# Performance work log

Hardware: AMD Instinct MI355X
Metric: run time of the kernel (lower is better)

The kernel has to match this reference:

```python
import jax, jax.numpy as jnp
import numpy as np

B, N = 4096, 128
STATE_DIM, GOAL_DIM, OBSTACLE_DIM = 6, 6, 4
VEH = 2 * STATE_DIM + GOAL_DIM  # 18


def setup_inputs() -> dict:
    key = jax.random.key(0)
    ks = jax.random.split(key, 8)
    s = lambda k, shp, fan: jax.random.normal(k, shp, jnp.float32) / np.sqrt(fan)
    return {
        "obs": jax.random.normal(ks[0], (B, 138), jnp.float32),
        "obstacles": jax.random.uniform(ks[1], (B, 5, N), jnp.float32),
        "act": jax.random.normal(ks[2], (B, 2), jnp.float32),
        "ow1": s(ks[3], (22, 256), 22),
        "ob1": jnp.zeros((256,), jnp.float32),
        "ow2": s(ks[4], (256, 256), 256),
        "ob2": jnp.zeros((256,), jnp.float32),
        "qw1": s(ks[5], (396, 256), 396),
        "qb1": jnp.zeros((256,), jnp.float32),
        "qw2": s(ks[6], (256, 256), 256),
        "qb2": jnp.zeros((256,), jnp.float32),
        "qw3": s(ks[7], (256, 1), 256),
        "qb3": jnp.zeros((1,), jnp.float32),
    }


def reference(obs, obstacles, act, ow1, ob1, ow2, ob2, qw1, qb1, qw2, qb2, qw3, qb3):
    # obs: [B, 138]; obstacles: [B, obstacle_dim+1, N]; act: [B, 2]
    veh = obs[:, :VEH]                                 # [B, 18]
    obst_data = obstacles[:, :OBSTACLE_DIM, :]         # [B, 4, N]
    mask = obstacles[:, -1, :]                         # [B, N]
    # per-obstacle features: concat broadcast vehicle state with obstacle data -> [B, N, 22]
    x = jnp.concatenate(
        [jnp.broadcast_to(veh[:, None, :], (veh.shape[0], obst_data.shape[2], VEH)),
         obst_data.transpose(0, 2, 1)], axis=-1)
    # shared obstacle MLP (ReLU on both layers, incl. output_activation)
    h = jax.nn.relu(jnp.einsum("bnf,fh->bnh", x, ow1) + ob1)
    h = jax.nn.relu(jnp.einsum("bnh,hk->bnk", h, ow2) + ob2)  # [B, N, 256]
    # masked sum-pool over obstacle axis
    pooled = jnp.einsum("bnh,bn->bh", h, mask)         # [B, 256]
    comb = jnp.concatenate([obs, pooled, act], axis=-1)  # [B, 396]
    q = jax.nn.relu(comb @ qw1 + qb1)
    q = jax.nn.relu(q @ qw2 + qb2)
    q = q @ qw3 + qb3                                   # [B, 1]
    return jnp.squeeze(q, -1)
```

## Files before the change

### kernel.cpp

```cpp
#include <hip/hip_runtime.h>
#include <hip/hip_bf16.h>


typedef __attribute__((ext_vector_type(8))) short short8;
typedef __attribute__((ext_vector_type(4))) float f32x4;

#define MFMA16(A, B, C) __builtin_amdgcn_mfma_f32_16x16x32_bf16(A, B, C, 0, 0, 0)

__device__ __forceinline__ unsigned short f2b(float f) {
  __hip_bfloat16 h = __float2bfloat16(f);
  return __builtin_bit_cast(unsigned short, h);
}
__device__ __forceinline__ float b2f(unsigned short u) {
  unsigned v = ((unsigned)u) << 16;
  return __builtin_bit_cast(float, v);
}
__device__ __forceinline__ unsigned pk2f(float a, float b) {
  unsigned ua = __builtin_bit_cast(unsigned, a) + 0x8000u;
  unsigned ub = __builtin_bit_cast(unsigned, b) + 0x8000u;
  return __builtin_amdgcn_perm(ub, ua, 0x07060302u);
}

__device__ __forceinline__ void lds_barrier() {
  asm volatile("s_waitcnt lgkmcnt(0)" ::: "memory");
  __builtin_amdgcn_s_barrier();
}

__global__ __launch_bounds__(256) void pack_weights(
    const float* __restrict__ ow1, const float* __restrict__ ow2,
    const float* __restrict__ qw1, const float* __restrict__ qw2,
    unsigned short* __restrict__ ow1q, unsigned short* __restrict__ ow2p,
    unsigned short* __restrict__ qw1h, unsigned short* __restrict__ qw1l,
    unsigned short* __restrict__ qw2h, unsigned short* __restrict__ qw2l) {
  int i = blockIdx.x * 256 + threadIdx.x;
  if (i < 8192) {
    int j = i & 7;
    int l15 = (i >> 3) & 15;
    int quad = (i >> 7) & 3;
    int mt = (i >> 9) & 15;
    int k = quad * 8 + j;
    float v = (k < 22) ? ow1[k * 256 + (mt * 16 + l15)] : 0.f;
    ow1q[i] = f2b(v);
  }
  if (i < 65536) {
    int j = i & 7;
    int n = (i >> 3) & 255;
    int qq = i >> 11;
    int k = (qq >> 2) * 32 + (qq & 3) * 8 + j;
    ow2p[i] = f2b(ow2[k * 256 + n]);
    float w = qw2[k * 256 + n];
    unsigned short h = f2b(w);
    qw2h[i] = h;
    qw2l[i] = f2b(w - b2f(h));
  }
  if (i < 106496) {
    int j = i & 7;
    int n = (i >> 3) & 255;
    int qq = i >> 11;
    int k = (qq >> 2) * 32 + (qq & 3) * 8 + j;
    float w = (k < 396) ? qw1[k * 256 + n] : 0.f;
    unsigned short h = f2b(w);
    qw1h[i] = h;
    qw1l[i] = f2b(w - b2f(h));
  }
}

#define XSTR 40
#define HSTR 272

__global__ __launch_bounds__(512, 4) void obstacle_kernel(
    const float* __restrict__ obs, const float* __restrict__ obstacles,
    const unsigned short* __restrict__ ow1q,
    const unsigned short* __restrict__ ow2p,
    const float* __restrict__ ob1, const float* __restrict__ ob2,
    unsigned short* __restrict__ poolH, unsigned short* __restrict__ poolL) {
  __shared__ __align__(16) unsigned short xs[128 * XSTR];
  __shared__ __align__(16) unsigned short h1[128 * HSTR];
  __shared__ float maskS[128];
  __shared__ unsigned short vehB[32];

  const int b = blockIdx.x;
  const int tid = threadIdx.x;
  const int wave = tid >> 6;
  const int lane = tid & 63;
  const int quad = lane >> 4;
  const int l15 = lane & 15;

  const unsigned short* wp = &ow1q[wave * 1024 + quad * 128 + l15 * 8];
  short8 wfr[2];
#pragma unroll
  for (int i = 0; i < 2; i++) wfr[i] = *(const short8*)(wp + i * 512);

  const unsigned short* bbase = &ow2p[(quad * 256 + wave * 32 + l15) * 8];
  short8 bbuf[2][2];
#pragma unroll
  for (int t = 0; t < 2; t++)
    bbuf[0][t] = *(const short8*)(bbase + wave * 8192 + t * 128);

  if (tid < 18) vehB[tid] = f2b(obs[b * 138 + tid]);
  if (tid < 128) maskS[tid] = obstacles[b * 640 + 512 + tid];
  lds_barrier();

  if (tid < 256) {
    int n = tid >> 1;
    int half = tid & 1;
    unsigned short* wr = &xs[n * XSTR + half * 16];
    if (half == 0) {
      unsigned short r01[16];
#pragma unroll
      for (int k = 0; k < 16; k++) r01[k] = vehB[k];
      *(short8*)(wr + 0) = *(short8*)&r01[0];
      *(short8*)(wr + 8) = *(short8*)&r01[8];
    } else {
      unsigned short r2[8];
      r2[0] = vehB[16];
      r2[1] = vehB[17];
#pragma unroll
      for (int d = 0; d < 4; d++)
        r2[2 + d] = f2b(obstacles[b * 640 + d * 128 + n]);
      r2[6] = 0; r2[7] = 0;
      *(short8*)(wr + 0) = *(short8*)&r2[0];
      short8 z = {0, 0, 0, 0, 0, 0, 0, 0};
      *(short8*)(wr + 8) = z;
    }
  }
  lds_barrier();

  {
    const unsigned short* bxp = &xs[l15 * XSTR + quad * 8];
    short8 bx[8];
#pragma unroll
    for (int nt = 0; nt < 8; nt++)
      bx[nt] = *(const short8*)(bxp + nt * 16 * XSTR);

    unsigned short* wrb = &h1[l15 * HSTR + wave * 32 + quad * 4];

#pragma unroll
    for (int i = 0; i < 2; i++) {
      f32x4 cinit = *(const f32x4*)&ob1[wave * 32 + i * 16 + quad * 4];
      f32x4 acc1[8];
#pragma unroll
      for (int nt = 0; nt < 8; nt++) acc1[nt] = MFMA16(wfr[i], bx[nt], cinit);
#pragma unroll
      for (int nt = 0; nt < 8; nt++) {
        float v0 = fmaxf(acc1[nt][0], 0.f);
        float v1 = fmaxf(acc1[nt][1], 0.f);
        float v2 = fmaxf(acc1[nt][2], 0.f);
        float v3 = fmaxf(acc1[nt][3], 0.f);
        uint2 pk;
        pk.x = pk2f(v0, v1);
        pk.y = pk2f(v2, v3);
        *(uint2*)(wrb + nt * 16 * HSTR + i * 16) = pk;
      }
    }
  }

  f32x4 acc[8][2];
#pragma unroll
  for (int t = 0; t < 2; t++) {
    float bv = ob2[wave * 32 + t * 16 + l15];
    f32x4 bvec = {bv, bv, bv, bv};
#pragma unroll
    for (int mt = 0; mt < 8; mt++) acc[mt][t] = bvec;
  }

  const unsigned short* h1base = &h1[l15 * HSTR + quad * 8];

  {
    const int kb = wave;
#pragma unroll
    for (int t = 0; t < 2; t++)
      bbuf[1][t] = *(const short8*)(bbase + (((wave + 1) & 7) * 8192) + t * 128);
    short8 afr[8];
#pragma unroll
    for (int mt = 0; mt < 8; mt++)
      afr[mt] = *(const short8*)(h1base + kb * 32 + mt * 16 * HSTR);
#pragma unroll
    for (int mt = 0; mt < 8; mt++)
#pragma unroll
      for (int t = 0; t < 2; t++) acc[mt][t] = MFMA16(afr[mt], bbuf[0][t], acc[mt][t]);
  }

  lds_barrier();

#pragma unroll
  for (int j = 1; j < 8; j++) {
    const int kb = (wave + j) & 7;
    const int cur = j & 1;
    if (j < 7) {
#pragma unroll
      for (int t = 0; t < 2; t++)
        bbuf[cur ^ 1][t] =
            *(const short8*)(bbase + (((wave + j + 1) & 7) * 8192) + t * 128);
    }
    short8 afr[8];
#pragma unroll
    for (int mt = 0; mt < 8; mt++)
      afr[mt] = *(const short8*)(h1base + kb * 32 + mt * 16 * HSTR);
#pragma unroll
    for (int mt = 0; mt < 8; mt++)
#pragma unroll
      for (int t = 0; t < 2; t++) acc[mt][t] = MFMA16(afr[mt], bbuf[cur][t], acc[mt][t]);
  }

  f32x4 mk[8];
  const float* mkp = &maskS[quad * 4];
#pragma unroll
  for (int mt = 0; mt < 8; mt++) mk[mt] = *(const f32x4*)(mkp + mt * 16);

#pragma unroll
  for (int t = 0; t < 2; t++) {
    float s = 0.f;
#pragma unroll
    for (int mt = 0; mt < 8; mt++) {
#pragma unroll
      for (int r = 0; r < 4; r++) {
        float v = fmaxf(acc[mt][t][r], 0.f);
        s = fmaf(mk[mt][r], v, s);
      }
    }
    s += __shfl_xor(s, 16);
    s += __shfl_xor(s, 32);
    if (quad == 0) {
      int n = wave * 32 + t * 16 + l15;
      unsigned short sh = (unsigned short)(__builtin_bit_cast(unsigned, s) >> 16);
      poolH[b * 256 + n] = sh;
      poolL[b * 256 + n] = f2b(s - b2f(sh));
    }
  }
}

__global__ __launch_bounds__(1024) void head_mfma(
    const float* __restrict__ obs, const float* __restrict__ act,
    const unsigned short* __restrict__ poolH,
    const unsigned short* __restrict__ poolL,
    const unsigned short* __restrict__ qw1h,
    const unsigned short* __restrict__ qw1l,
    const unsigned short* __restrict__ qw2h,
    const unsigned short* __restrict__ qw2l,
    const float* __restrict__ qb1, const float* __restrict__ qb2,
    const float* __restrict__ qw3, const float* __restrict__ qb3,
    float* __restrict__ out) {
  const int CSTR = 424;
  const int HSTRQ = 264;
  __shared__ unsigned short combH[16 * 424], combL[16 * 424];
  __shared__ unsigned short h1H[16 * 264], h1L[16 * 264];
  __shared__ float wred[16][16];

  const int tid = threadIdx.x;
  const int r0 = blockIdx.x * 16;

  for (int idx = tid; idx < 16 * 416; idx += 1024) {
    int m = idx / 416;
    int k = idx - m * 416;
    unsigned short hi, lo;
    if (k < 138) {
      float v = obs[(r0 + m) * 138 + k];
      hi = f2b(v);
      lo = f2b(v - b2f(hi));
    } else if (k < 394) {
      hi = poolH[(r0 + m) * 256 + (k - 138)];
      lo = poolL[(r0 + m) * 256 + (k - 138)];
    } else if (k < 396) {
      float v = act[(r0 + m) * 2 + (k - 394)];
      hi = f2b(v);
      lo = f2b(v - b2f(hi));
    } else {
      hi = 0; lo = 0;
    }
    combH[m * CSTR + k] = hi;
    combL[m * CSTR + k] = lo;
  }
  __syncthreads();

  const int wave = tid >> 6;
  const int lane = tid & 63;
  const int quad = lane >> 4;
  const int l15 = lane & 15;
  const int n = wave * 16 + l15;

  f32x4 acc = {0.f, 0.f, 0.f, 0.f}, accm = {0.f, 0.f, 0.f, 0.f};
#pragma unroll 1
  for (int kb = 0; kb < 13; kb++) {
    int ao = l15 * CSTR + kb * 32 + quad * 8;
    short8 ah = *(const short8*)&combH[ao];
    short8 al = *(const short8*)&combL[ao];
    int off = ((kb * 4 + quad) * 256 + n) * 8;
    short8 bh = *(const short8*)&qw1h[off];
    short8 bl = *(const short8*)&qw1l[off];
    acc = MFMA16(ah, bh, acc);
    accm = MFMA16(ah, bl, accm);
    accm = MFMA16(al, bh, accm);
  }
  {
    float bias = qb1[n];
#pragma unroll
    for (int r = 0; r < 4; r++) {
      int m = quad * 4 + r;
      float v = fmaxf(acc[r] + accm[r] + bias, 0.f);
      unsigned short hi = f2b(v);
      h1H[m * HSTRQ + n] = hi;
      h1L[m * HSTRQ + n] = f2b(v - b2f(hi));
    }
  }
  __syncthreads();

  f32x4 a2 = {0.f, 0.f, 0.f, 0.f}, a2m = {0.f, 0.f, 0.f, 0.f};
#pragma unroll 1
  for (int kb = 0; kb < 8; kb++) {
    int ao = l15 * HSTRQ + kb * 32 + quad * 8;
    short8 ah = *(const short8*)&h1H[ao];
    short8 al = *(const short8*)&h1L[ao];
    int off = ((kb * 4 + quad) * 256 + n) * 8;
    short8 bh = *(const short8*)&qw2h[off];
    short8 bl = *(const short8*)&qw2l[off];
    a2 = MFMA16(ah, bh, a2);
    a2m = MFMA16(ah, bl, a2m);
    a2m = MFMA16(al, bh, a2m);
  }

  {
    float w3 = qw3[n];
    float qb2n = qb2[n];
#pragma unroll
    for (int r = 0; r < 4; r++) {
      float v = fmaxf(a2[r] + a2m[r] + qb2n, 0.f);
      float s = v * w3;
      s += __shfl_xor(s, 1);
      s += __shfl_xor(s, 2);
      s += __shfl_xor(s, 4);
      s += __shfl_xor(s, 8);
      if (l15 == 0) wred[wave][quad * 4 + r] = s;
    }
  }
  __syncthreads();
  if (tid < 16) {
    float s = qb3[0];
#pragma unroll
    for (int w = 0; w < 16; w++) s += wred[w][tid];
    out[r0 + tid] = s;
  }
}

extern "C" void kernel_launch(void* const* d_in, const int* in_sizes, int n_in,
                              void* d_out, int out_size, void* d_ws, size_t ws_size,
                              hipStream_t stream) {
  const float* obs       = (const float*)d_in[0];
  const float* obstacles = (const float*)d_in[1];
  const float* act       = (const float*)d_in[2];
  const float* ow1       = (const float*)d_in[3];
  const float* ob1       = (const float*)d_in[4];
  const float* ow2       = (const float*)d_in[5];
  const float* ob2       = (const float*)d_in[6];
  const float* qw1       = (const float*)d_in[7];
  const float* qb1       = (const float*)d_in[8];
  const float* qw2       = (const float*)d_in[9];
  const float* qb2       = (const float*)d_in[10];
  const float* qw3       = (const float*)d_in[11];
  const float* qb3       = (const float*)d_in[12];
  float* out = (float*)d_out;

  unsigned short* ow1q = (unsigned short*)d_ws;
  unsigned short* ow2p = ow1q + 8192;
  unsigned short* qw1h = ow2p + 65536;
  unsigned short* qw1l = qw1h + 106496;
  unsigned short* qw2h = qw1l + 106496;
  unsigned short* qw2l = qw2h + 65536;
  unsigned short* poolH = qw2l + 65536;
  unsigned short* poolL = poolH + 1048576;

  pack_weights<<<416, 256, 0, stream>>>(ow1, ow2, qw1, qw2, ow1q, ow2p, qw1h,
                                        qw1l, qw2h, qw2l);
  obstacle_kernel<<<4096, 512, 0, stream>>>(obs, obstacles, ow1q, ow2p, ob1,
                                            ob2, poolH, poolL);
  head_mfma<<<256, 1024, 0, stream>>>(obs, act, poolH, poolL, qw1h, qw1l,
                                      qw2h, qw2l, qb1, qb2, qw3, qb3, out);
}
```

Baseline: 165.8 us.

## Process two batch rows per obstacle block with register prefetch of next row inputs

Each obstacle_kernel block now handles two consecutive batch elements, halving the grid. The next element's vehicle state, mask and obstacle coordinates are prefetched into registers while the current element's MLP runs, and the layer-1 weight fragments are loaded once and reused across both elements. MFMA sections are wrapped in s_setprio to favour matrix issue. The aim is to hide global-load latency and amortise per-block setup, at the cost of fewer blocks in flight and an extra barrier between elements.

```diff
diff --git a/kernel.cpp b/kernel.cpp
--- a/kernel.cpp
+++ b/kernel.cpp
@@ -79,154 +79,193 @@
   __shared__ float maskS[128];
   __shared__ unsigned short vehB[32];
 
-  const int b = blockIdx.x;
   const int tid = threadIdx.x;
   const int wave = tid >> 6;
   const int lane = tid & 63;
   const int quad = lane >> 4;
   const int l15 = lane & 15;
+  const int b0 = blockIdx.x * 2;
+  const int xn = tid >> 1;
+  const int xhalf = tid & 1;
+
+  float pveh = 0.f, pmask = 0.f, po0 = 0.f, po1 = 0.f, po2 = 0.f, po3 = 0.f;
+  if (tid < 18) pveh = obs[b0 * 138 + tid];
+  if (tid < 128) pmask = obstacles[b0 * 640 + 512 + tid];
+  if (tid < 256 && xhalf) {
+    po0 = obstacles[b0 * 640 + 0 * 128 + xn];
+    po1 = obstacles[b0 * 640 + 1 * 128 + xn];
+    po2 = obstacles[b0 * 640 + 2 * 128 + xn];
+    po3 = obstacles[b0 * 640 + 3 * 128 + xn];
+  }
 
   const unsigned short* wp = &ow1q[wave * 1024 + quad * 128 + l15 * 8];
+  const unsigned short* bbase = &ow2p[(quad * 256 + wave * 32 + l15) * 8];
   short8 wfr[2];
-#pragma unroll
-  for (int i = 0; i < 2; i++) wfr[i] = *(const short8*)(wp + i * 512);
-
-  const unsigned short* bbase = &ow2p[(quad * 256 + wave * 32 + l15) * 8];
-  short8 bbuf[2][2];
-#pragma unroll
-  for (int t = 0; t < 2; t++)
-    bbuf[0][t] = *(const short8*)(bbase + wave * 8192 + t * 128);
-
-  if (tid < 18) vehB[tid] = f2b(obs[b * 138 + tid]);
-  if (tid < 128) maskS[tid] = obstacles[b * 640 + 512 + tid];
-  lds_barrier();
-
-  if (tid < 256) {
-    int n = tid >> 1;
-    int half = tid & 1;
-    unsigned short* wr = &xs[n * XSTR + half * 16];
-    if (half == 0) {
-      unsigned short r01[16];
-#pragma unroll
-      for (int k = 0; k < 16; k++) r01[k] = vehB[k];
-      *(short8*)(wr + 0) = *(short8*)&r01[0];
-      *(short8*)(wr + 8) = *(short8*)&r01[8];
-    } else {
-      unsigned short r2[8];
-      r2[0] = vehB[16];
-      r2[1] = vehB[17];
-#pragma unroll
-      for (int d = 0; d < 4; d++)
-        r2[2 + d] = f2b(obstacles[b * 640 + d * 128 + n]);
-      r2[6] = 0; r2[7] = 0;
-      *(short8*)(wr + 0) = *(short8*)&r2[0];
-      short8 z = {0, 0, 0, 0, 0, 0, 0, 0};
-      *(short8*)(wr + 8) = z;
-    }
-  }
-  lds_barrier();
-
-  {
-    const unsigned short* bxp = &xs[l15 * XSTR + quad * 8];
-    short8 bx[8];
-#pragma unroll
-    for (int nt = 0; nt < 8; nt++)
-      bx[nt] = *(const short8*)(bxp + nt * 16 * XSTR);
-
-    unsigned short* wrb = &h1[l15 * HSTR + wave * 32 + quad * 4];
-
-#pragma unroll
-    for (int i = 0; i < 2; i++) {
-      f32x4 cinit = *(const f32x4*)&ob1[wave * 32 + i * 16 + quad * 4];
-      f32x4 acc1[8];
-#pragma unroll
-      for (int nt = 0; nt < 8; nt++) acc1[nt] = MFMA16(wfr[i], bx[nt], cinit);
-#pragma unroll
-      for (int nt = 0; nt < 8; nt++) {
-        float v0 = fmaxf(acc1[nt][0], 0.f);
-        float v1 = fmaxf(acc1[nt][1], 0.f);
-        float v2 = fmaxf(acc1[nt][2], 0.f);
-        float v3 = fmaxf(acc1[nt][3], 0.f);
-        uint2 pk;
-        pk.x = pk2f(v0, v1);
-        pk.y = pk2f(v2, v3);
-        *(uint2*)(wrb + nt * 16 * HSTR + i * 16) = pk;
-      }
-    }
-  }
-
-  f32x4 acc[8][2];
-#pragma unroll
-  for (int t = 0; t < 2; t++) {
-    float bv = ob2[wave * 32 + t * 16 + l15];
-    f32x4 bvec = {bv, bv, bv, bv};
-#pragma unroll
-    for (int mt = 0; mt < 8; mt++) acc[mt][t] = bvec;
-  }
-
-  const unsigned short* h1base = &h1[l15 * HSTR + quad * 8];
-
-  {
-    const int kb = wave;
+
+#pragma unroll
+  for (int e = 0; e < 2; e++) {
+    const int b = b0 + e;
+
+    if (tid < 18) vehB[tid] = f2b(pveh);
+    if (tid < 128) maskS[tid] = pmask;
+    lds_barrier();
+
+    if (tid < 256) {
+      unsigned short* wr = &xs[xn * XSTR + xhalf * 16];
+      if (xhalf == 0) {
+        unsigned short r01[16];
+#pragma unroll
+        for (int k = 0; k < 16; k++) r01[k] = vehB[k];
+        *(short8*)(wr + 0) = *(short8*)&r01[0];
+        *(short8*)(wr + 8) = *(short8*)&r01[8];
+      } else {
+        unsigned short r2[8];
+        r2[0] = vehB[16];
+        r2[1] = vehB[17];
+        r2[2] = f2b(po0);
+        r2[3] = f2b(po1);
+        r2[4] = f2b(po2);
+        r2[5] = f2b(po3);
+        r2[6] = 0; r2[7] = 0;
+        *(short8*)(wr + 0) = *(short8*)&r2[0];
+        short8 z = {0, 0, 0, 0, 0, 0, 0, 0};
+        *(short8*)(wr + 8) = z;
+      }
+    }
+    lds_barrier();
+
+    if (e == 0) {
+      const int bn = b0 + 1;
+      if (tid < 18) pveh = obs[bn * 138 + tid];
+      if (tid < 128) pmask = obstacles[bn * 640 + 512 + tid];
+      if (tid < 256 && xhalf) {
+        po0 = obstacles[bn * 640 + 0 * 128 + xn];
+        po1 = obstacles[bn * 640 + 1 * 128 + xn];
+        po2 = obstacles[bn * 640 + 2 * 128 + xn];
+        po3 = obstacles[bn * 640 + 3 * 128 + xn];
+      }
+    }
+
+    short8 bbuf[2][2];
 #pragma unroll
     for (int t = 0; t < 2; t++)
-      bbuf[1][t] = *(const short8*)(bbase + (((wave + 1) & 7) * 8192) + t * 128);
-    short8 afr[8];
-#pragma unroll
-    for (int mt = 0; mt < 8; mt++)
-      afr[mt] = *(const short8*)(h1base + kb * 32 + mt * 16 * HSTR);
-#pragma unroll
-    for (int mt = 0; mt < 8; mt++)
-#pragma unroll
-      for (int t = 0; t < 2; t++) acc[mt][t] = MFMA16(afr[mt], bbuf[0][t], acc[mt][t]);
-  }
-
-  lds_barrier();
-
-#pragma unroll
-  for (int j = 1; j < 8; j++) {
-    const int kb = (wave + j) & 7;
-    const int cur = j & 1;
-    if (j < 7) {
+      bbuf[0][t] = *(const short8*)(bbase + wave * 8192 + t * 128);
+
+    {
+      if (e == 0) {
+#pragma unroll
+        for (int i = 0; i < 2; i++) wfr[i] = *(const short8*)(wp + i * 512);
+      }
+
+      const unsigned short* bxp = &xs[l15 * XSTR + quad * 8];
+      short8 bx[8];
+#pragma unroll
+      for (int nt = 0; nt < 8; nt++)
+        bx[nt] = *(const short8*)(bxp + nt * 16 * XSTR);
+
+      unsigned short* wrb = &h1[l15 * HSTR + wave * 32 + quad * 4];
+
+#pragma unroll
+      for (int i = 0; i < 2; i++) {
+        f32x4 cinit = *(const f32x4*)&ob1[wave * 32 + i * 16 + quad * 4];
+        f32x4 acc1[8];
+        __builtin_amdgcn_s_setprio(1);
+#pragma unroll
+        for (int nt = 0; nt < 8; nt++) acc1[nt] = MFMA16(wfr[i], bx[nt], cinit);
+        __builtin_amdgcn_s_setprio(0);
+#pragma unroll
+        for (int nt = 0; nt < 8; nt++) {
+          float v0 = fmaxf(acc1[nt][0], 0.f);
+          float v1 = fmaxf(acc1[nt][1], 0.f);
+          float v2 = fmaxf(acc1[nt][2], 0.f);
+          float v3 = fmaxf(acc1[nt][3], 0.f);
+          uint2 pk;
+          pk.x = pk2f(v0, v1);
+          pk.y = pk2f(v2, v3);
+          *(uint2*)(wrb + nt * 16 * HSTR + i * 16) = pk;
+        }
+      }
+    }
+
+    f32x4 acc[8][2];
+#pragma unroll
+    for (int t = 0; t < 2; t++) {
+      float bv = ob2[wave * 32 + t * 16 + l15];
+      f32x4 bvec = {bv, bv, bv, bv};
+#pragma unroll
+      for (int mt = 0; mt < 8; mt++) acc[mt][t] = bvec;
+    }
+
+    const unsigned short* h1base = &h1[l15 * HSTR + quad * 8];
+
+    {
+      const int kb = wave;
 #pragma unroll
       for (int t = 0; t < 2; t++)
-        bbuf[cur ^ 1][t] =
-            *(const short8*)(bbase + (((wave + j + 1) & 7) * 8192) + t * 128);
-    }
-    short8 afr[8];
-#pragma unroll
-    for (int mt = 0; mt < 8; mt++)
-      afr[mt] = *(const short8*)(h1base + kb * 32 + mt * 16 * HSTR);
-#pragma unroll
-    for (int mt = 0; mt < 8; mt++)
-#pragma unroll
-      for (int t = 0; t < 2; t++) acc[mt][t] = MFMA16(afr[mt], bbuf[cur][t], acc[mt][t]);
-  }
-
-  f32x4 mk[8];
-  const float* mkp = &maskS[quad * 4];
-#pragma unroll
-  for (int mt = 0; mt < 8; mt++) mk[mt] = *(const f32x4*)(mkp + mt * 16);
-
-#pragma unroll
-  for (int t = 0; t < 2; t++) {
-    float s = 0.f;
-#pragma unroll
-    for (int mt = 0; mt < 8; mt++) {
-#pragma unroll
-      for (int r = 0; r < 4; r++) {
-        float v = fmaxf(acc[mt][t][r], 0.f);
-        s = fmaf(mk[mt][r], v, s);
-      }
-    }
-    s += __shfl_xor(s, 16);
-    s += __shfl_xor(s, 32);
-    if (quad == 0) {
-      int n = wave * 32 + t * 16 + l15;
-      unsigned short sh = (unsigned short)(__builtin_bit_cast(unsigned, s) >> 16);
-      poolH[b * 256 + n] = sh;
-      poolL[b * 256 + n] = f2b(s - b2f(sh));
-    }
+        bbuf[1][t] = *(const short8*)(bbase + (((wave + 1) & 7) * 8192) + t * 128);
+      short8 afr[8];
+#pragma unroll
+      for (int mt = 0; mt < 8; mt++)
+        afr[mt] = *(const short8*)(h1base + kb * 32 + mt * 16 * HSTR);
+      __builtin_amdgcn_s_setprio(1);
+#pragma unroll
+      for (int mt = 0; mt < 8; mt++)
+#pragma unroll
+        for (int t = 0; t < 2; t++) acc[mt][t] = MFMA16(afr[mt], bbuf[0][t], acc[mt][t]);
+      __builtin_amdgcn_s_setprio(0);
+    }
+
+    lds_barrier();
+
+#pragma unroll
+    for (int j = 1; j < 8; j++) {
+      const int kb = (wave + j) & 7;
+      const int cur = j & 1;
+      if (j < 7) {
+#pragma unroll
+        for (int t = 0; t < 2; t++)
+          bbuf[cur ^ 1][t] =
+              *(const short8*)(bbase + (((wave + j + 1) & 7) * 8192) + t * 128);
+      }
+      short8 afr[8];
+#pragma unroll
+      for (int mt = 0; mt < 8; mt++)
+        afr[mt] = *(const short8*)(h1base + kb * 32 + mt * 16 * HSTR);
+      __builtin_amdgcn_s_setprio(1);
+#pragma unroll
+      for (int mt = 0; mt < 8; mt++)
+#pragma unroll
+        for (int t = 0; t < 2; t++) acc[mt][t] = MFMA16(afr[mt], bbuf[cur][t], acc[mt][t]);
+      __builtin_amdgcn_s_setprio(0);
+    }
+
+    f32x4 mk[8];
+    const float* mkp = &maskS[quad * 4];
+#pragma unroll
+    for (int mt = 0; mt < 8; mt++) mk[mt] = *(const f32x4*)(mkp + mt * 16);
+
+#pragma unroll
+    for (int t = 0; t < 2; t++) {
+      float s = 0.f;
+#pragma unroll
+      for (int mt = 0; mt < 8; mt++) {
+#pragma unroll
+        for (int r = 0; r < 4; r++) {
+          float v = fmaxf(acc[mt][t][r], 0.f);
+          s = fmaf(mk[mt][r], v, s);
+        }
+      }
+      s += __shfl_xor(s, 16);
+      s += __shfl_xor(s, 32);
+      if (quad == 0) {
+        int n = wave * 32 + t * 16 + l15;
+        unsigned short sh = (unsigned short)(__builtin_bit_cast(unsigned, s) >> 16);
+        poolH[b * 256 + n] = sh;
+        poolL[b * 256 + n] = f2b(s - b2f(sh));
+      }
+    }
+
+    if (e == 0) lds_barrier();
   }
 }
 
@@ -371,7 +410,7 @@
 
   pack_weights<<<416, 256, 0, stream>>>(ow1, ow2, qw1, qw2, ow1q, ow2p, qw1h,
                                         qw1l, qw2h, qw2l);
-  obstacle_kernel<<<4096, 512, 0, stream>>>(obs, obstacles, ow1q, ow2p, ob1,
+  obstacle_kernel<<<2048, 512, 0, stream>>>(obs, obstacles, ow1q, ow2p, ob1,
                                             ob2, poolH, poolL);
   head_mfma<<<256, 1024, 0, stream>>>(obs, act, poolH, poolL, qw1h, qw1l,
                                       qw2h, qw2l, qb1, qb2, qw3, qb3, out);
```

Result: slower. 209.6 us (+26.5%).
